# Kernel tuning notes

Hardware: AMD Instinct MI355X
Metric: run time of the kernel (lower is better)

The kernel has to match this reference:

```python
import jax, jax.numpy as jnp
import numpy as np

NEG_INF = -9.0e15  # matches torch's -9000000000000000.0 mask value
ALPHA = 0.2        # LeakyReLU negative slope from init_kwargs


def setup_inputs() -> dict:
    key = jax.random.key(0)
    k1, k2, k3, k4, k5 = jax.random.split(key, 5)
    B, N, D, A = 64, 128, 128, 1000
    hidden = jax.random.normal(k1, (B, N, D), dtype=jnp.float32)
    adj = jax.random.randint(k2, (B, N, N), 0, 5)  # edge types 0..4 (0 = masked)
    a = jax.random.normal(k3, (D, 4), dtype=jnp.float32) * 0.1  # stacked a_0..a_3
    A_attr_sess = jax.random.uniform(k4, (B, N, A), dtype=jnp.float32)
    attr_embedding = jax.random.normal(k5, (A, D), dtype=jnp.float32)
    return {"hidden": hidden, "adj": adj, "a": a,
            "A_attr_sess": A_attr_sess, "attr_embedding": attr_embedding}


def reference(hidden, adj, a, A_attr_sess, attr_embedding):
    # a_input[b,i,j,:] = leaky_relu(h[b,i,:] * h[b,j,:])  -> [B,N,N,D]
    a_input = jax.nn.leaky_relu(hidden[:, :, None, :] * hidden[:, None, :, :],
                                negative_slope=ALPHA)
    # four edge-type scores in one contraction: [B,N,N,4]
    e = jnp.einsum('bijd,dk->bijk', a_input, a)
    # masked selection by adjacency edge type (later writes override earlier)
    alpha = jnp.full(adj.shape, NEG_INF, dtype=e.dtype)
    alpha = jnp.where(adj == 1, e[..., 0], alpha)
    alpha = jnp.where(adj == 2, e[..., 1], alpha)
    alpha = jnp.where(adj == 3, e[..., 2], alpha)
    alpha = jnp.where(adj == 4, e[..., 3], alpha)
    attn = jax.nn.softmax(alpha, axis=-1)        # [B,N,N]
    output = jnp.einsum('bij,bjd->bid', attn, hidden)  # [B,N,D]
    attr_sess = jnp.einsum('bna,ad->bnd', A_attr_sess, attr_embedding)
    return output, attr_sess
```

## Files before the change

### kernel.cpp

```cpp
#include <hip/hip_runtime.h>

#define BB 64
#define NN 128
#define DD 128
#define AA 1000
#define KPAD 1024
#define NEG_INF (-9.0e15f)

typedef __attribute__((ext_vector_type(8))) short short8;
typedef __attribute__((ext_vector_type(4))) float floatx4;
typedef __attribute__((ext_vector_type(4))) unsigned int uintx4;
typedef __attribute__((ext_vector_type(2))) unsigned int uintx2;

__device__ __forceinline__ float bflo(unsigned int u) { return __uint_as_float(u << 16); }
__device__ __forceinline__ float bfhi(unsigned int u) { return __uint_as_float(u & 0xffff0000u); }
__device__ __forceinline__ unsigned int packbf(float f0, float f1) {
  return (__float_as_uint(f0) >> 16) | (__float_as_uint(f1) & 0xffff0000u);
}
__device__ __forceinline__ unsigned short bf_rne(float f) {
  unsigned int u = __float_as_uint(f);
  return (unsigned short)((u + 0x7fffu + ((u >> 16) & 1u)) >> 16);
}
__device__ __forceinline__ unsigned int packbf_rne(float f0, float f1) {
  return (unsigned int)bf_rne(f0) | ((unsigned int)bf_rne(f1) << 16);
}
__device__ __forceinline__ short8 u2s(uintx4 v) {
  union { uintx4 u; short8 s; } x; x.u = v; return x.s;
}

__global__ __launch_bounds__(256) void prep_kernel(
    const float* __restrict__ hidden, const float* __restrict__ emb,
    unsigned short* __restrict__ ET, unsigned short* __restrict__ HTg)
{
  __shared__ float hsf[NN * 129];
  const int t = threadIdx.x;
  const int bid = blockIdx.x;
  if (bid < BB) {
    const float* hb = hidden + (size_t)bid * NN * DD;
    #pragma unroll
    for (int u = 0; u < 16; ++u) {
      int e = u * 1024 + t * 4;
      float4 v = *reinterpret_cast<const float4*>(hb + e);
      int r = e >> 7, c = e & 127;
      float* d = &hsf[r * 129 + c];
      d[0] = v.x; d[1] = v.y; d[2] = v.z; d[3] = v.w;
    }
    __syncthreads();
    unsigned short* ht16 = HTg + (size_t)bid * NN * DD;
    #pragma unroll
    for (int u = 0; u < 8; ++u) {
      int e = u * 2048 + t * 8;
      int dI = e >> 7, il = e & 127;
      float x[8];
      #pragma unroll
      for (int j = 0; j < 8; ++j) x[j] = hsf[(il + j) * 129 + dI];
      uintx4 o;
      o.x = packbf_rne(x[0], x[1]); o.y = packbf_rne(x[2], x[3]);
      o.z = packbf_rne(x[4], x[5]); o.w = packbf_rne(x[6], x[7]);
      *reinterpret_cast<uintx4*>(ht16 + e) = o;
    }
  } else {
    const int k0 = (bid - BB) * 32;
    #pragma unroll
    for (int u = 0; u < 4; ++u) {
      int e = u * 1024 + t * 4;
      int r = e >> 7, c = e & 127;
      float4 z = {0.f, 0.f, 0.f, 0.f};
      float4 v = (k0 + r < AA)
          ? *reinterpret_cast<const float4*>(emb + (size_t)(k0 + r) * DD + c) : z;
      float* d = &hsf[r * 129 + c];
      d[0] = v.x; d[1] = v.y; d[2] = v.z; d[3] = v.w;
    }
    __syncthreads();
    int c = t >> 1, j0 = (t & 1) * 16;
    float x[16];
    #pragma unroll
    for (int j = 0; j < 16; ++j) x[j] = hsf[(j0 + j) * 129 + c];
    uintx4 o0, o1;
    o0.x = packbf_rne(x[0], x[1]);  o0.y = packbf_rne(x[2], x[3]);
    o0.z = packbf_rne(x[4], x[5]);  o0.w = packbf_rne(x[6], x[7]);
    o1.x = packbf_rne(x[8], x[9]);  o1.y = packbf_rne(x[10], x[11]);
    o1.z = packbf_rne(x[12], x[13]); o1.w = packbf_rne(x[14], x[15]);
    unsigned short* dst = ET + (size_t)c * KPAD + k0 + j0;
    *reinterpret_cast<uintx4*>(dst) = o0;
    *reinterpret_cast<uintx4*>(dst + 8) = o1;
  }
}

struct AttnSmem {
  __align__(16) unsigned short Hs[NN * 128];
  union {
    __align__(16) unsigned short As[4 * 16 * 256];
    struct {
      __align__(16) float Sa[16 * 129];
      __align__(16) unsigned short W[16 * 128];
    } sw;
  } u2;
  __align__(16) float saf[4 * 256];
};

#define BK 64
struct AttrSmem {
  __align__(16) unsigned short ETs[2][DD * BK];
  __align__(16) unsigned short As2[2][16 * BK];
};

union FusedSmem { AttnSmem a; AttrSmem g; };

__device__ __forceinline__ void attn_body(
    AttnSmem& s, const float* __restrict__ hidden,
    const int* __restrict__ adj, const float* __restrict__ amat,
    const unsigned short* __restrict__ HTg, float* __restrict__ out0,
    int wid)
{
  const int t = threadIdx.x;
  const int L = t & 63, w = t >> 6;
  const int lr = L & 15, lq = L >> 4;
  const int b = wid >> 3;
  const int i0 = (wid & 7) * 16;

  const int* adjb = adj + ((size_t)b * NN + i0) * NN;
  int adjv[8];
  #pragma unroll
  for (int nt = 0; nt < 2; ++nt)
    #pragma unroll
    for (int r = 0; r < 4; ++r)
      adjv[nt * 4 + r] = adjb[(lq * 4 + r) * NN + w * 32 + nt * 16 + lr];

  const float* hb = hidden + (size_t)b * NN * DD;
  #pragma unroll
  for (int u = 0; u < 8; ++u) {
    int id = u * 256 + t;
    int r = id >> 4, c = id & 15;
    const float* src = hb + r * 128 + c * 8;
    float4 v0 = *reinterpret_cast<const float4*>(src);
    float4 v1 = *reinterpret_cast<const float4*>(src + 4);
    uintx4 o;
    o.x = packbf_rne(v0.x, v0.y); o.y = packbf_rne(v0.z, v0.w);
    o.z = packbf_rne(v1.x, v1.y); o.w = packbf_rne(v1.z, v1.w);
    *reinterpret_cast<uintx4*>(&s.Hs[r * 128 + ((c ^ (r & 15)) << 3)]) = o;
  }
  {
    float v1 = amat[t], v2 = amat[t + 256];
    int dI = t >> 2, k = t & 3;
    s.saf[k * 256 + dI] = 0.6f * v1;
    s.saf[k * 256 + 128 + dI] = 0.4f * v1;
    s.saf[k * 256 + 64 + dI] = 0.6f * v2;
    s.saf[k * 256 + 192 + dI] = 0.4f * v2;
  }
  __syncthreads();

  #pragma unroll
  for (int u = 0; u < 8; ++u) {
    int id = u * 256 + t;
    int k = id >> 9, ii = (id >> 5) & 15, c = id & 31;
    int srow = i0 + ii;
    int dchunk = c & 15;
    uintx4 hv = *reinterpret_cast<const uintx4*>(
        &s.Hs[srow * 128 + ((dchunk ^ (srow & 15)) << 3)]);
    if (c & 16) {
      hv.x &= 0x7fff7fffu; hv.y &= 0x7fff7fffu;
      hv.z &= 0x7fff7fffu; hv.w &= 0x7fff7fffu;
    }
    const float* sf = &s.saf[k * 256 + c * 8];
    uintx4 o;
    o.x = packbf(bflo(hv.x) * sf[0], bfhi(hv.x) * sf[1]);
    o.y = packbf(bflo(hv.y) * sf[2], bfhi(hv.y) * sf[3]);
    o.z = packbf(bflo(hv.z) * sf[4], bfhi(hv.z) * sf[5]);
    o.w = packbf(bflo(hv.w) * sf[6], bfhi(hv.w) * sf[7]);
    *reinterpret_cast<uintx4*>(&s.u2.As[k * 4096 + ii * 256 + ((c ^ ii) << 3)]) = o;
  }
  __syncthreads();

  floatx4 acc[4][2];
  #pragma unroll
  for (int k = 0; k < 4; ++k)
    #pragma unroll
    for (int nt = 0; nt < 2; ++nt) acc[k][nt] = floatx4{0.f, 0.f, 0.f, 0.f};

  #pragma unroll
  for (int kt = 0; kt < 8; ++kt) {
    int ca = lq + 4 * kt;
    short8 afr[4];
    #pragma unroll
    for (int k = 0; k < 4; ++k)
      afr[k] = *reinterpret_cast<const short8*>(
          &s.u2.As[k * 4096 + lr * 256 + ((ca ^ lr) << 3)]);
    int cb = lq + 4 * (kt & 3);
    short8 bfr[2];
    #pragma unroll
    for (int nt = 0; nt < 2; ++nt) {
      int jrow = w * 32 + nt * 16 + lr;
      uintx4 hv = *reinterpret_cast<const uintx4*>(
          &s.Hs[jrow * 128 + ((cb ^ (jrow & 15)) << 3)]);
      if (kt >= 4) {
        hv.x &= 0x7fff7fffu; hv.y &= 0x7fff7fffu;
        hv.z &= 0x7fff7fffu; hv.w &= 0x7fff7fffu;
      }
      bfr[nt] = u2s(hv);
    }
    #pragma unroll
    for (int k = 0; k < 4; ++k)
      #pragma unroll
      for (int nt = 0; nt < 2; ++nt)
        acc[k][nt] = __builtin_amdgcn_mfma_f32_16x16x32_bf16(
            afr[k], bfr[nt], acc[k][nt], 0, 0, 0);
  }
  __syncthreads();

  short8 pvb[2][4];
  const unsigned short* ht = HTg + (size_t)b * NN * DD;
  #pragma unroll
  for (int nt = 0; nt < 2; ++nt)
    #pragma unroll
    for (int kt = 0; kt < 4; ++kt) {
      int dI = w * 32 + nt * 16 + lr;
      pvb[nt][kt] = *reinterpret_cast<const short8*>(ht + dI * 128 + kt * 32 + lq * 8);
    }

  #pragma unroll
  for (int nt = 0; nt < 2; ++nt)
    #pragma unroll
    for (int r = 0; r < 4; ++r) {
      int ii = lq * 4 + r;
      int j = w * 32 + nt * 16 + lr;
      int ad = adjv[nt * 4 + r];
      float al = NEG_INF;
      al = (ad == 1) ? acc[0][nt][r] : al;
      al = (ad == 2) ? acc[1][nt][r] : al;
      al = (ad == 3) ? acc[2][nt][r] : al;
      al = (ad == 4) ? acc[3][nt][r] : al;
      s.u2.sw.Sa[ii * 129 + j] = al;
    }
  __syncthreads();

  #pragma unroll
  for (int p = 0; p < 4; ++p) {
    int ii = w * 4 + p;
    float a1 = s.u2.sw.Sa[ii * 129 + L];
    float a2 = s.u2.sw.Sa[ii * 129 + 64 + L];
    float m = fmaxf(a1, a2);
    #pragma unroll
    for (int off = 32; off > 0; off >>= 1) m = fmaxf(m, __shfl_xor(m, off, 64));
    float e1 = __expf(fmaxf(a1 - m, -80.f));
    float e2 = __expf(fmaxf(a2 - m, -80.f));
    float ss = e1 + e2;
    #pragma unroll
    for (int off = 32; off > 0; off >>= 1) ss += __shfl_xor(ss, off, 64);
    float inv = 1.f / ss;
    int j2 = L + 64;
    s.u2.sw.W[ii * 128 + (((L >> 3) ^ ii) << 3) + (L & 7)] = bf_rne(e1 * inv);
    s.u2.sw.W[ii * 128 + (((j2 >> 3) ^ ii) << 3) + (j2 & 7)] = bf_rne(e2 * inv);
  }
  __syncthreads();

  floatx4 oacc[2];
  oacc[0] = floatx4{0.f, 0.f, 0.f, 0.f};
  oacc[1] = floatx4{0.f, 0.f, 0.f, 0.f};
  #pragma unroll
  for (int kt = 0; kt < 4; ++kt) {
    int c = lq + 4 * kt;
    short8 wf = *reinterpret_cast<const short8*>(
        &s.u2.sw.W[lr * 128 + ((c ^ lr) << 3)]);
    #pragma unroll
    for (int nt = 0; nt < 2; ++nt)
      oacc[nt] = __builtin_amdgcn_mfma_f32_16x16x32_bf16(
          wf, pvb[nt][kt], oacc[nt], 0, 0, 0);
  }
  float* ob = out0 + ((size_t)b * NN + i0) * DD;
  #pragma unroll
  for (int nt = 0; nt < 2; ++nt)
    #pragma unroll
    for (int r = 0; r < 4; ++r)
      ob[(lq * 4 + r) * DD + w * 32 + nt * 16 + lr] = oacc[nt][r];
}

__device__ __forceinline__ void attr_body(
    AttrSmem& s, const float* __restrict__ Aattr,
    const unsigned short* __restrict__ ET, float* __restrict__ out1,
    int wid)
{
  const int t = threadIdx.x;
  const int L = t & 63, w = t >> 6;
  const int lr = L & 15, lq = L >> 4;
  const int r0 = wid * 16;

  const int ar = t >> 4;
  const int ak = (t & 15) * 4;
  const int ec = t >> 1, ej0 = (t & 1) * 4;
  const float* arow = Aattr + (size_t)(r0 + ar) * AA;
  const unsigned short* erow = ET + (size_t)ec * KPAD;

  float4 paA, paB;
  uintx4 peA[4], peB[4];

#define ATTR_FETCH(PA, PE, IT) do {                                          \
    int kb = (IT) * BK; int k4 = kb + ak;                                    \
    float4 z = {0.f, 0.f, 0.f, 0.f};                                        \
    PA = (k4 < AA) ? *reinterpret_cast<const float4*>(arow + k4) : z;        \
    _Pragma("unroll")                                                        \
    for (int q = 0; q < 4; ++q)                                              \
      PE[q] = *reinterpret_cast<const uintx4*>(erow + kb + (ej0 + q) * 8);   \
  } while (0)

#define ATTR_STAGE(PA, PE, BUF) do {                                         \
    uintx2 o; o.x = packbf(PA.x, PA.y); o.y = packbf(PA.z, PA.w);            \
    int cidx = ak >> 3, half = ak & 7;                                       \
    *reinterpret_cast<uintx2*>(                                              \
        &s.As2[BUF][ar * BK + ((cidx ^ (ar & 7)) << 3) + half]) = o;         \
    _Pragma("unroll")                                                        \
    for (int q = 0; q < 4; ++q)                                              \
      *reinterpret_cast<uintx4*>(                                            \
          &s.ETs[BUF][ec * BK + (((ej0 + q) ^ (ec & 7)) << 3)]) = PE[q];     \
  } while (0)

#define ATTR_COMPUTE(BUF) do {                                               \
    _Pragma("unroll")                                                        \
    for (int ks = 0; ks < 2; ++ks) {                                         \
      int c = lq + 4 * ks;                                                   \
      short8 af = *reinterpret_cast<const short8*>(                          \
          &s.As2[BUF][lr * BK + ((c ^ (lr & 7)) << 3)]);                     \
      _Pragma("unroll")                                                      \
      for (int nt = 0; nt < 2; ++nt) {                                       \
        int n = w * 32 + nt * 16 + lr;                                       \
        short8 bf = *reinterpret_cast<const short8*>(                        \
            &s.ETs[BUF][n * BK + ((c ^ (n & 7)) << 3)]);                     \
        acc[nt] = __builtin_amdgcn_mfma_f32_16x16x32_bf16(                   \
            af, bf, acc[nt], 0, 0, 0);                                       \
      }                                                                      \
    }                                                                        \
  } while (0)

  floatx4 acc[2];
  acc[0] = floatx4{0.f, 0.f, 0.f, 0.f};
  acc[1] = floatx4{0.f, 0.f, 0.f, 0.f};

  ATTR_FETCH(paA, peA, 0);
  ATTR_FETCH(paB, peB, 1);
  for (int ith = 0; ith < 8; ++ith) {
    ATTR_STAGE(paA, peA, 0);
    __syncthreads();
    if (ith < 7) ATTR_FETCH(paA, peA, 2 * ith + 2);
    ATTR_COMPUTE(0);
    ATTR_STAGE(paB, peB, 1);
    __syncthreads();
    if (ith < 7) ATTR_FETCH(paB, peB, 2 * ith + 3);
    ATTR_COMPUTE(1);
  }
#undef ATTR_FETCH
#undef ATTR_STAGE
#undef ATTR_COMPUTE

  float* ob = out1 + (size_t)r0 * DD;
  #pragma unroll
  for (int nt = 0; nt < 2; ++nt)
    #pragma unroll
    for (int r = 0; r < 4; ++r)
      ob[(lq * 4 + r) * DD + w * 32 + nt * 16 + lr] = acc[nt][r];
}

__global__ __launch_bounds__(256, 2) void fused_kernel(
    const float* __restrict__ hidden, const int* __restrict__ adj,
    const float* __restrict__ amat, const float* __restrict__ Aattr,
    const unsigned short* __restrict__ ET, const unsigned short* __restrict__ HTg,
    float* __restrict__ out0, float* __restrict__ out1)
{
  __shared__ FusedSmem sm;
  const int bid = blockIdx.x;
  const int wid = (bid & 7) * 64 + (bid >> 3);
  if (wid & 1) {
    attn_body(sm.a, hidden, adj, amat, HTg, out0, wid);
    __syncthreads();
    attr_body(sm.g, Aattr, ET, out1, wid);
  } else {
    attr_body(sm.g, Aattr, ET, out1, wid);
    __syncthreads();
    attn_body(sm.a, hidden, adj, amat, HTg, out0, wid);
  }
}

extern "C" void kernel_launch(void* const* d_in, const int* in_sizes, int n_in,
                              void* d_out, int out_size, void* d_ws, size_t ws_size,
                              hipStream_t stream) {
  const float* hidden = (const float*)d_in[0];
  const int*   adj    = (const int*)d_in[1];
  const float* amat   = (const float*)d_in[2];
  const float* Aattr  = (const float*)d_in[3];
  const float* emb    = (const float*)d_in[4];

  float* out0 = (float*)d_out;
  float* out1 = out0 + (size_t)BB * NN * DD;

  unsigned short* ET  = (unsigned short*)d_ws;
  unsigned short* HTg = ET + (size_t)DD * KPAD;

  prep_kernel<<<BB + 32, 256, 0, stream>>>(hidden, emb, ET, HTg);
  fused_kernel<<<512, 256, 0, stream>>>(hidden, adj, amat, Aattr, ET, HTg,
                                        out0, out1);
}
```

Before: 104.4 us.

## Split attention and attr GEMM into separate blocks, shrink LDS, pre-swizzle bf16 hidden

The prep kernel now also writes a bf16, pre-swizzled copy of hidden, so attention blocks copy it straight into LDS instead of converting fp32 on the fly. The attention score scratch is halved by processing the four edge-type A-operands in two passes, and B fragments are held in registers across both passes. The attr GEMM now computes 32 rows per block with wider A loads. The fused kernel launches 768 single-purpose blocks instead of 512 blocks that each ran both bodies in sequence. Less LDS and launch_bounds of 3 aim to raise occupancy, at the cost of an extra workspace buffer, more global writes in prep, and an extra barrier in the attention pass.

```diff
diff --git a/kernel.cpp b/kernel.cpp
--- a/kernel.cpp
+++ b/kernel.cpp
@@ -30,7 +30,8 @@
 
 __global__ __launch_bounds__(256) void prep_kernel(
     const float* __restrict__ hidden, const float* __restrict__ emb,
-    unsigned short* __restrict__ ET, unsigned short* __restrict__ HTg)
+    unsigned short* __restrict__ ET, unsigned short* __restrict__ HTg,
+    unsigned short* __restrict__ Hg)
 {
   __shared__ float hsf[NN * 129];
   const int t = threadIdx.x;
@@ -59,6 +60,17 @@
       o.z = packbf_rne(x[4], x[5]); o.w = packbf_rne(x[6], x[7]);
       *reinterpret_cast<uintx4*>(ht16 + e) = o;
     }
+    unsigned short* hg = Hg + (size_t)bid * NN * DD;
+    #pragma unroll
+    for (int u = 0; u < 8; ++u) {
+      int id = u * 256 + t;
+      int r = id >> 4, c = id & 15;
+      const float* src = &hsf[r * 129 + c * 8];
+      uintx4 o;
+      o.x = packbf_rne(src[0], src[1]); o.y = packbf_rne(src[2], src[3]);
+      o.z = packbf_rne(src[4], src[5]); o.w = packbf_rne(src[6], src[7]);
+      *reinterpret_cast<uintx4*>(&hg[r * 128 + ((c ^ (r & 15)) << 3)]) = o;
+    }
   } else {
     const int k0 = (bid - BB) * 32;
     #pragma unroll
@@ -90,7 +102,7 @@
 struct AttnSmem {
   __align__(16) unsigned short Hs[NN * 128];
   union {
-    __align__(16) unsigned short As[4 * 16 * 256];
+    __align__(16) unsigned short As[2 * 16 * 256];
     struct {
       __align__(16) float Sa[16 * 129];
       __align__(16) unsigned short W[16 * 128];
@@ -102,22 +114,21 @@
 #define BK 64
 struct AttrSmem {
   __align__(16) unsigned short ETs[2][DD * BK];
-  __align__(16) unsigned short As2[2][16 * BK];
+  __align__(16) unsigned short As2[2][32 * BK];
 };
 
 union FusedSmem { AttnSmem a; AttrSmem g; };
 
 __device__ __forceinline__ void attn_body(
-    AttnSmem& s, const float* __restrict__ hidden,
-    const int* __restrict__ adj, const float* __restrict__ amat,
-    const unsigned short* __restrict__ HTg, float* __restrict__ out0,
-    int wid)
+    AttnSmem& s, const int* __restrict__ adj, const float* __restrict__ amat,
+    const unsigned short* __restrict__ Hg, const unsigned short* __restrict__ HTg,
+    float* __restrict__ out0, int tile)
 {
   const int t = threadIdx.x;
   const int L = t & 63, w = t >> 6;
   const int lr = L & 15, lq = L >> 4;
-  const int b = wid >> 3;
-  const int i0 = (wid & 7) * 16;
+  const int b = tile >> 3;
+  const int i0 = (tile & 7) * 16;
 
   const int* adjb = adj + ((size_t)b * NN + i0) * NN;
   int adjv[8];
@@ -127,18 +138,12 @@
     for (int r = 0; r < 4; ++r)
       adjv[nt * 4 + r] = adjb[(lq * 4 + r) * NN + w * 32 + nt * 16 + lr];
 
-  const float* hb = hidden + (size_t)b * NN * DD;
+  const unsigned short* hg = Hg + (size_t)b * NN * DD;
   #pragma unroll
   for (int u = 0; u < 8; ++u) {
     int id = u * 256 + t;
-    int r = id >> 4, c = id & 15;
-    const float* src = hb + r * 128 + c * 8;
-    float4 v0 = *reinterpret_cast<const float4*>(src);
-    float4 v1 = *reinterpret_cast<const float4*>(src + 4);
-    uintx4 o;
-    o.x = packbf_rne(v0.x, v0.y); o.y = packbf_rne(v0.z, v0.w);
-    o.z = packbf_rne(v1.x, v1.y); o.w = packbf_rne(v1.z, v1.w);
-    *reinterpret_cast<uintx4*>(&s.Hs[r * 128 + ((c ^ (r & 15)) << 3)]) = o;
+    *reinterpret_cast<uintx4*>(&s.Hs[id * 8]) =
+        *reinterpret_cast<const uintx4*>(hg + id * 8);
   }
   {
     float v1 = amat[t], v2 = amat[t + 256];
@@ -150,27 +155,15 @@
   }
   __syncthreads();
 
-  #pragma unroll
-  for (int u = 0; u < 8; ++u) {
-    int id = u * 256 + t;
-    int k = id >> 9, ii = (id >> 5) & 15, c = id & 31;
-    int srow = i0 + ii;
-    int dchunk = c & 15;
-    uintx4 hv = *reinterpret_cast<const uintx4*>(
-        &s.Hs[srow * 128 + ((dchunk ^ (srow & 15)) << 3)]);
-    if (c & 16) {
-      hv.x &= 0x7fff7fffu; hv.y &= 0x7fff7fffu;
-      hv.z &= 0x7fff7fffu; hv.w &= 0x7fff7fffu;
-    }
-    const float* sf = &s.saf[k * 256 + c * 8];
-    uintx4 o;
-    o.x = packbf(bflo(hv.x) * sf[0], bfhi(hv.x) * sf[1]);
-    o.y = packbf(bflo(hv.y) * sf[2], bfhi(hv.y) * sf[3]);
-    o.z = packbf(bflo(hv.z) * sf[4], bfhi(hv.z) * sf[5]);
-    o.w = packbf(bflo(hv.w) * sf[6], bfhi(hv.w) * sf[7]);
-    *reinterpret_cast<uintx4*>(&s.u2.As[k * 4096 + ii * 256 + ((c ^ ii) << 3)]) = o;
-  }
-  __syncthreads();
+  uintx4 hvq[2][4];
+  #pragma unroll
+  for (int nt = 0; nt < 2; ++nt)
+    #pragma unroll
+    for (int q = 0; q < 4; ++q) {
+      int jrow = w * 32 + nt * 16 + lr;
+      hvq[nt][q] = *reinterpret_cast<const uintx4*>(
+          &s.Hs[jrow * 128 + (((lq + 4 * q) ^ (jrow & 15)) << 3)]);
+    }
 
   floatx4 acc[4][2];
   #pragma unroll
@@ -179,32 +172,52 @@
     for (int nt = 0; nt < 2; ++nt) acc[k][nt] = floatx4{0.f, 0.f, 0.f, 0.f};
 
   #pragma unroll
-  for (int kt = 0; kt < 8; ++kt) {
-    int ca = lq + 4 * kt;
-    short8 afr[4];
-    #pragma unroll
-    for (int k = 0; k < 4; ++k)
-      afr[k] = *reinterpret_cast<const short8*>(
-          &s.u2.As[k * 4096 + lr * 256 + ((ca ^ lr) << 3)]);
-    int cb = lq + 4 * (kt & 3);
-    short8 bfr[2];
-    #pragma unroll
-    for (int nt = 0; nt < 2; ++nt) {
-      int jrow = w * 32 + nt * 16 + lr;
+  for (int kp = 0; kp < 2; ++kp) {
+    if (kp) __syncthreads();
+    #pragma unroll
+    for (int u = 0; u < 4; ++u) {
+      int id = u * 256 + t;
+      int kk = id >> 9, ii = (id >> 5) & 15, c = id & 31;
+      int srow = i0 + ii;
+      int dchunk = c & 15;
       uintx4 hv = *reinterpret_cast<const uintx4*>(
-          &s.Hs[jrow * 128 + ((cb ^ (jrow & 15)) << 3)]);
-      if (kt >= 4) {
+          &s.Hs[srow * 128 + ((dchunk ^ (srow & 15)) << 3)]);
+      if (c & 16) {
         hv.x &= 0x7fff7fffu; hv.y &= 0x7fff7fffu;
         hv.z &= 0x7fff7fffu; hv.w &= 0x7fff7fffu;
       }
-      bfr[nt] = u2s(hv);
-    }
-    #pragma unroll
-    for (int k = 0; k < 4; ++k)
+      const float* sf = &s.saf[(kp * 2 + kk) * 256 + c * 8];
+      uintx4 o;
+      o.x = packbf(bflo(hv.x) * sf[0], bfhi(hv.x) * sf[1]);
+      o.y = packbf(bflo(hv.y) * sf[2], bfhi(hv.y) * sf[3]);
+      o.z = packbf(bflo(hv.z) * sf[4], bfhi(hv.z) * sf[5]);
+      o.w = packbf(bflo(hv.w) * sf[6], bfhi(hv.w) * sf[7]);
+      *reinterpret_cast<uintx4*>(&s.u2.As[kk * 4096 + ii * 256 + ((c ^ ii) << 3)]) = o;
+    }
+    __syncthreads();
+
+    #pragma unroll
+    for (int kt = 0; kt < 8; ++kt) {
+      int ca = lq + 4 * kt;
+      short8 afr[2];
       #pragma unroll
-      for (int nt = 0; nt < 2; ++nt)
-        acc[k][nt] = __builtin_amdgcn_mfma_f32_16x16x32_bf16(
-            afr[k], bfr[nt], acc[k][nt], 0, 0, 0);
+      for (int kk = 0; kk < 2; ++kk)
+        afr[kk] = *reinterpret_cast<const short8*>(
+            &s.u2.As[kk * 4096 + lr * 256 + ((ca ^ lr) << 3)]);
+      #pragma unroll
+      for (int nt = 0; nt < 2; ++nt) {
+        uintx4 hv = hvq[nt][kt & 3];
+        if (kt >= 4) {
+          hv.x &= 0x7fff7fffu; hv.y &= 0x7fff7fffu;
+          hv.z &= 0x7fff7fffu; hv.w &= 0x7fff7fffu;
+        }
+        short8 bfr = u2s(hv);
+        #pragma unroll
+        for (int kk = 0; kk < 2; ++kk)
+          acc[kp * 2 + kk][nt] = __builtin_amdgcn_mfma_f32_16x16x32_bf16(
+              afr[kk], bfr, acc[kp * 2 + kk][nt], 0, 0, 0);
+      }
+    }
   }
   __syncthreads();
 
@@ -277,37 +290,39 @@
 
 __device__ __forceinline__ void attr_body(
     AttrSmem& s, const float* __restrict__ Aattr,
-    const unsigned short* __restrict__ ET, float* __restrict__ out1,
-    int wid)
+    const unsigned short* __restrict__ ET, float* __restrict__ out1, int tile)
 {
   const int t = threadIdx.x;
   const int L = t & 63, w = t >> 6;
   const int lr = L & 15, lq = L >> 4;
-  const int r0 = wid * 16;
-
-  const int ar = t >> 4;
-  const int ak = (t & 15) * 4;
+  const int r0 = tile * 32;
+
+  const int ar = t >> 3;
+  const int ak = (t & 7) * 8;
   const int ec = t >> 1, ej0 = (t & 1) * 4;
   const float* arow = Aattr + (size_t)(r0 + ar) * AA;
   const unsigned short* erow = ET + (size_t)ec * KPAD;
 
-  float4 paA, paB;
+  float4 pa0A, pa1A, pa0B, pa1B;
   uintx4 peA[4], peB[4];
 
-#define ATTR_FETCH(PA, PE, IT) do {                                          \
+#define ATTR_FETCH(P0, P1, PE, IT) do {                                      \
     int kb = (IT) * BK; int k4 = kb + ak;                                    \
     float4 z = {0.f, 0.f, 0.f, 0.f};                                        \
-    PA = (k4 < AA) ? *reinterpret_cast<const float4*>(arow + k4) : z;        \
+    P0 = (k4 < AA) ? *reinterpret_cast<const float4*>(arow + k4) : z;        \
+    P1 = (k4 + 4 < AA) ? *reinterpret_cast<const float4*>(arow + k4 + 4) : z;\
     _Pragma("unroll")                                                        \
     for (int q = 0; q < 4; ++q)                                              \
       PE[q] = *reinterpret_cast<const uintx4*>(erow + kb + (ej0 + q) * 8);   \
   } while (0)
 
-#define ATTR_STAGE(PA, PE, BUF) do {                                         \
-    uintx2 o; o.x = packbf(PA.x, PA.y); o.y = packbf(PA.z, PA.w);            \
-    int cidx = ak >> 3, half = ak & 7;                                       \
-    *reinterpret_cast<uintx2*>(                                              \
-        &s.As2[BUF][ar * BK + ((cidx ^ (ar & 7)) << 3) + half]) = o;         \
+#define ATTR_STAGE(P0, P1, PE, BUF) do {                                     \
+    uintx4 o;                                                                \
+    o.x = packbf(P0.x, P0.y); o.y = packbf(P0.z, P0.w);                      \
+    o.z = packbf(P1.x, P1.y); o.w = packbf(P1.z, P1.w);                      \
+    int ac = t & 7;                                                          \
+    *reinterpret_cast<uintx4*>(                                              \
+        &s.As2[BUF][ar * BK + ((ac ^ (ar & 7)) << 3)]) = o;                  \
     _Pragma("unroll")                                                        \
     for (int q = 0; q < 4; ++q)                                              \
       *reinterpret_cast<uintx4*>(                                            \
@@ -318,33 +333,44 @@
     _Pragma("unroll")                                                        \
     for (int ks = 0; ks < 2; ++ks) {                                         \
       int c = lq + 4 * ks;                                                   \
-      short8 af = *reinterpret_cast<const short8*>(                          \
-          &s.As2[BUF][lr * BK + ((c ^ (lr & 7)) << 3)]);                     \
+      short8 af[2], bf[2];                                                   \
+      _Pragma("unroll")                                                      \
+      for (int mt = 0; mt < 2; ++mt) {                                       \
+        int row = mt * 16 + lr;                                              \
+        af[mt] = *reinterpret_cast<const short8*>(                           \
+            &s.As2[BUF][row * BK + ((c ^ (row & 7)) << 3)]);                 \
+      }                                                                      \
       _Pragma("unroll")                                                      \
       for (int nt = 0; nt < 2; ++nt) {                                       \
         int n = w * 32 + nt * 16 + lr;                                       \
-        short8 bf = *reinterpret_cast<const short8*>(                        \
+        bf[nt] = *reinterpret_cast<const short8*>(                           \
             &s.ETs[BUF][n * BK + ((c ^ (n & 7)) << 3)]);                     \
-        acc[nt] = __builtin_amdgcn_mfma_f32_16x16x32_bf16(                   \
-            af, bf, acc[nt], 0, 0, 0);                                       \
       }                                                                      \
+      _Pragma("unroll")                                                      \
+      for (int mt = 0; mt < 2; ++mt)                                         \
+        _Pragma("unroll")                                                    \
+        for (int nt = 0; nt < 2; ++nt)                                       \
+          acc[mt][nt] = __builtin_amdgcn_mfma_f32_16x16x32_bf16(             \
+              af[mt], bf[nt], acc[mt][nt], 0, 0, 0);                         \
     }                                                                        \
   } while (0)
 
-  floatx4 acc[2];
-  acc[0] = floatx4{0.f, 0.f, 0.f, 0.f};
-  acc[1] = floatx4{0.f, 0.f, 0.f, 0.f};
-
-  ATTR_FETCH(paA, peA, 0);
-  ATTR_FETCH(paB, peB, 1);
+  floatx4 acc[2][2];
+  #pragma unroll
+  for (int mt = 0; mt < 2; ++mt)
+    #pragma unroll
+    for (int nt = 0; nt < 2; ++nt) acc[mt][nt] = floatx4{0.f, 0.f, 0.f, 0.f};
+
+  ATTR_FETCH(pa0A, pa1A, peA, 0);
+  ATTR_FETCH(pa0B, pa1B, peB, 1);
   for (int ith = 0; ith < 8; ++ith) {
-    ATTR_STAGE(paA, peA, 0);
+    ATTR_STAGE(pa0A, pa1A, peA, 0);
     __syncthreads();
-    if (ith < 7) ATTR_FETCH(paA, peA, 2 * ith + 2);
+    if (ith < 7) ATTR_FETCH(pa0A, pa1A, peA, 2 * ith + 2);
     ATTR_COMPUTE(0);
-    ATTR_STAGE(paB, peB, 1);
+    ATTR_STAGE(pa0B, pa1B, peB, 1);
     __syncthreads();
-    if (ith < 7) ATTR_FETCH(paB, peB, 2 * ith + 3);
+    if (ith < 7) ATTR_FETCH(pa0B, pa1B, peB, 2 * ith + 3);
     ATTR_COMPUTE(1);
   }
 #undef ATTR_FETCH
@@ -353,30 +379,26 @@
 
   float* ob = out1 + (size_t)r0 * DD;
   #pragma unroll
-  for (int nt = 0; nt < 2; ++nt)
-    #pragma unroll
-    for (int r = 0; r < 4; ++r)
-      ob[(lq * 4 + r) * DD + w * 32 + nt * 16 + lr] = acc[nt][r];
-}
-
-__global__ __launch_bounds__(256, 2) void fused_kernel(
-    const float* __restrict__ hidden, const int* __restrict__ adj,
-    const float* __restrict__ amat, const float* __restrict__ Aattr,
-    const unsigned short* __restrict__ ET, const unsigned short* __restrict__ HTg,
+  for (int mt = 0; mt < 2; ++mt)
+    #pragma unroll
+    for (int nt = 0; nt < 2; ++nt)
+      #pragma unroll
+      for (int r = 0; r < 4; ++r)
+        ob[(mt * 16 + lq * 4 + r) * DD + w * 32 + nt * 16 + lr] = acc[mt][nt][r];
+}
+
+__global__ __launch_bounds__(256, 3) void fused_kernel(
+    const int* __restrict__ adj, const float* __restrict__ amat,
+    const float* __restrict__ Aattr, const unsigned short* __restrict__ ET,
+    const unsigned short* __restrict__ HTg, const unsigned short* __restrict__ Hg,
     float* __restrict__ out0, float* __restrict__ out1)
 {
   __shared__ FusedSmem sm;
   const int bid = blockIdx.x;
-  const int wid = (bid & 7) * 64 + (bid >> 3);
-  if (wid & 1) {
-    attn_body(sm.a, hidden, adj, amat, HTg, out0, wid);
-    __syncthreads();
-    attr_body(sm.g, Aattr, ET, out1, wid);
-  } else {
-    attr_body(sm.g, Aattr, ET, out1, wid);
-    __syncthreads();
-    attn_body(sm.a, hidden, adj, amat, HTg, out0, wid);
-  }
+  const int wid = (bid & 7) * 96 + (bid >> 3);
+  const int m3 = wid % 3;
+  if (m3 == 2) attr_body(sm.g, Aattr, ET, out1, wid / 3);
+  else         attn_body(sm.a, adj, amat, Hg, HTg, out0, (wid / 3) * 2 + m3);
 }
 
 extern "C" void kernel_launch(void* const* d_in, const int* in_sizes, int n_in,
@@ -393,8 +415,9 @@
 
   unsigned short* ET  = (unsigned short*)d_ws;
   unsigned short* HTg = ET + (size_t)DD * KPAD;
-
-  prep_kernel<<<BB + 32, 256, 0, stream>>>(hidden, emb, ET, HTg);
-  fused_kernel<<<512, 256, 0, stream>>>(hidden, adj, amat, Aattr, ET, HTg,
+  unsigned short* Hg  = HTg + (size_t)BB * NN * DD;
+
+  prep_kernel<<<BB + 32, 256, 0, stream>>>(hidden, emb, ET, HTg, Hg);
+  fused_kernel<<<768, 256, 0, stream>>>(adj, amat, Aattr, ET, HTg, Hg,
                                         out0, out1);
 }
```

Measured after the change: 105.4 us. No clear change (+1.0%).

## Interleave attention phases into attr GEMM pipeline slots with merged shared memory

Applied to the files above, without the earlier changes.

Fuses the two previously serial bodies into one kernel that interleaves attention phases (As build, QK MFMA, select, softmax, PV) between the K-loop stages of the attribute GEMM. The aim is to hide global-load latency and keep the MFMA units busy. Each block now handles 32 attention rows and 32 attr rows, so the grid halves to 256 blocks at one block per CU. Shared memory is merged rather than unioned, which raises LDS use and register pressure, and fewer resident waves could lower latency hiding.

```diff
diff --git a/kernel.cpp b/kernel.cpp
--- a/kernel.cpp
+++ b/kernel.cpp
@@ -5,6 +5,7 @@
 #define DD 128
 #define AA 1000
 #define KPAD 1024
+#define BK 64
 #define NEG_INF (-9.0e15f)
 
 typedef __attribute__((ext_vector_type(8))) short short8;
@@ -87,58 +88,267 @@
   }
 }
 
-struct AttnSmem {
+struct MergedSmem {
   __align__(16) unsigned short Hs[NN * 128];
   union {
-    __align__(16) unsigned short As[4 * 16 * 256];
+    __align__(16) unsigned short As[2 * 16 * 256];
     struct {
       __align__(16) float Sa[16 * 129];
       __align__(16) unsigned short W[16 * 128];
     } sw;
   } u2;
   __align__(16) float saf[4 * 256];
+  __align__(16) unsigned short ETs[2][DD * BK];
+  __align__(16) unsigned short As2[2][32 * BK];
 };
 
-#define BK 64
-struct AttrSmem {
-  __align__(16) unsigned short ETs[2][DD * BK];
-  __align__(16) unsigned short As2[2][16 * BK];
-};
-
-union FusedSmem { AttnSmem a; AttrSmem g; };
-
-__device__ __forceinline__ void attn_body(
-    AttnSmem& s, const float* __restrict__ hidden,
-    const int* __restrict__ adj, const float* __restrict__ amat,
-    const unsigned short* __restrict__ HTg, float* __restrict__ out0,
-    int wid)
+__global__ __launch_bounds__(256, 1) void fused_kernel(
+    const float* __restrict__ hidden, const int* __restrict__ adj,
+    const float* __restrict__ amat, const float* __restrict__ Aattr,
+    const unsigned short* __restrict__ ET, const unsigned short* __restrict__ HTg,
+    float* __restrict__ out0, float* __restrict__ out1)
 {
+  __shared__ MergedSmem s;
   const int t = threadIdx.x;
   const int L = t & 63, w = t >> 6;
   const int lr = L & 15, lq = L >> 4;
-  const int b = wid >> 3;
-  const int i0 = (wid & 7) * 16;
-
-  const int* adjb = adj + ((size_t)b * NN + i0) * NN;
-  int adjv[8];
+  const int bid = blockIdx.x;
+  const int wid = (bid & 7) * 32 + (bid >> 3);
+  const int b = wid >> 2;
+  const int i0A = (wid & 3) * 32;
+  const int i0B = i0A + 16;
+  const int r0 = wid * 32;
+
+  const int ar = t >> 3, ak = (t & 7) * 8;
+  const int ec = t >> 1, ej0 = (t & 1) * 4;
+  const float* arow = Aattr + (size_t)(r0 + ar) * AA;
+  const unsigned short* erow = ET + (size_t)ec * KPAD;
+  float4 pa0[2], pa1[2];
+  uintx4 pe[2][4];
+  floatx4 acc2[2][2];
+  #pragma unroll
+  for (int mt = 0; mt < 2; ++mt)
+    #pragma unroll
+    for (int nt = 0; nt < 2; ++nt) acc2[mt][nt] = floatx4{0.f, 0.f, 0.f, 0.f};
+
+#define AFETCH(SP, IT) do {                                                  \
+    int kb = (IT) * BK; int k4 = kb + ak;                                    \
+    float4 z = {0.f, 0.f, 0.f, 0.f};                                        \
+    pa0[SP] = (k4 < AA) ? *reinterpret_cast<const float4*>(arow + k4) : z;   \
+    pa1[SP] = (k4 + 4 < AA) ? *reinterpret_cast<const float4*>(arow + k4 + 4) : z; \
+    _Pragma("unroll")                                                        \
+    for (int q = 0; q < 4; ++q)                                              \
+      pe[SP][q] = *reinterpret_cast<const uintx4*>(erow + kb + (ej0 + q) * 8); \
+  } while (0)
+
+#define ASTAGE(SP) do {                                                      \
+    uintx4 o;                                                                \
+    o.x = packbf(pa0[SP].x, pa0[SP].y); o.y = packbf(pa0[SP].z, pa0[SP].w);  \
+    o.z = packbf(pa1[SP].x, pa1[SP].y); o.w = packbf(pa1[SP].z, pa1[SP].w);  \
+    int ac = t & 7;                                                          \
+    *reinterpret_cast<uintx4*>(&s.As2[SP][ar * BK + ((ac ^ (ar & 7)) << 3)]) = o; \
+    _Pragma("unroll")                                                        \
+    for (int q = 0; q < 4; ++q)                                              \
+      *reinterpret_cast<uintx4*>(&s.ETs[SP][ec * BK + (((ej0 + q) ^ (ec & 7)) << 3)]) = pe[SP][q]; \
+  } while (0)
+
+#define ACOMPUTE(SP) do {                                                    \
+    _Pragma("unroll")                                                        \
+    for (int ks = 0; ks < 2; ++ks) {                                         \
+      int c = lq + 4 * ks;                                                   \
+      short8 af[2], bfv[2];                                                  \
+      _Pragma("unroll")                                                      \
+      for (int mt = 0; mt < 2; ++mt) {                                       \
+        int row = mt * 16 + lr;                                              \
+        af[mt] = *reinterpret_cast<const short8*>(                           \
+            &s.As2[SP][row * BK + ((c ^ (row & 7)) << 3)]);                  \
+      }                                                                      \
+      _Pragma("unroll")                                                      \
+      for (int nt = 0; nt < 2; ++nt) {                                       \
+        int n = w * 32 + nt * 16 + lr;                                       \
+        bfv[nt] = *reinterpret_cast<const short8*>(                          \
+            &s.ETs[SP][n * BK + ((c ^ (n & 7)) << 3)]);                      \
+      }                                                                      \
+      _Pragma("unroll")                                                      \
+      for (int mt = 0; mt < 2; ++mt)                                         \
+        _Pragma("unroll")                                                    \
+        for (int nt = 0; nt < 2; ++nt)                                       \
+          acc2[mt][nt] = __builtin_amdgcn_mfma_f32_16x16x32_bf16(            \
+              af[mt], bfv[nt], acc2[mt][nt], 0, 0, 0);                       \
+    }                                                                        \
+  } while (0)
+
+  floatx4 acc[4][2];
+  uintx4 hvq[2][4];
+  short8 pvb[2][4];
+
+#define ZACC do {                                                            \
+    _Pragma("unroll")                                                        \
+    for (int k = 0; k < 4; ++k)                                              \
+      _Pragma("unroll")                                                      \
+      for (int nt = 0; nt < 2; ++nt) acc[k][nt] = floatx4{0.f, 0.f, 0.f, 0.f}; \
+  } while (0)
+
+#define HVQHOIST do {                                                        \
+    _Pragma("unroll")                                                        \
+    for (int nt = 0; nt < 2; ++nt)                                           \
+      _Pragma("unroll")                                                      \
+      for (int q = 0; q < 4; ++q) {                                          \
+        int jrow = w * 32 + nt * 16 + lr;                                    \
+        hvq[nt][q] = *reinterpret_cast<const uintx4*>(                       \
+            &s.Hs[jrow * 128 + (((lq + 4 * q) ^ (jrow & 15)) << 3)]);        \
+      }                                                                      \
+  } while (0)
+
+#define ASBUILD(I0, KP) do {                                                 \
+    _Pragma("unroll")                                                        \
+    for (int u = 0; u < 4; ++u) {                                            \
+      int id = u * 256 + t;                                                  \
+      int kk = id >> 9, ii = (id >> 5) & 15, c = id & 31;                    \
+      int srow = (I0) + ii;                                                  \
+      int dchunk = c & 15;                                                   \
+      uintx4 hv = *reinterpret_cast<const uintx4*>(                          \
+          &s.Hs[srow * 128 + ((dchunk ^ (srow & 15)) << 3)]);                \
+      if (c & 16) {                                                          \
+        hv.x &= 0x7fff7fffu; hv.y &= 0x7fff7fffu;                            \
+        hv.z &= 0x7fff7fffu; hv.w &= 0x7fff7fffu;                            \
+      }                                                                      \
+      const float* sf = &s.saf[((KP) * 2 + kk) * 256 + c * 8];               \
+      uintx4 o;                                                              \
+      o.x = packbf(bflo(hv.x) * sf[0], bfhi(hv.x) * sf[1]);                  \
+      o.y = packbf(bflo(hv.y) * sf[2], bfhi(hv.y) * sf[3]);                  \
+      o.z = packbf(bflo(hv.z) * sf[4], bfhi(hv.z) * sf[5]);                  \
+      o.w = packbf(bflo(hv.w) * sf[6], bfhi(hv.w) * sf[7]);                  \
+      *reinterpret_cast<uintx4*>(&s.u2.As[kk * 4096 + ii * 256 + ((c ^ ii) << 3)]) = o; \
+    }                                                                        \
+  } while (0)
+
+#define QKPASS(KP) do {                                                      \
+    _Pragma("unroll")                                                        \
+    for (int kt2 = 0; kt2 < 8; ++kt2) {                                      \
+      int ca = lq + 4 * kt2;                                                 \
+      short8 afr[2];                                                         \
+      _Pragma("unroll")                                                      \
+      for (int kk = 0; kk < 2; ++kk)                                         \
+        afr[kk] = *reinterpret_cast<const short8*>(                          \
+            &s.u2.As[kk * 4096 + lr * 256 + ((ca ^ lr) << 3)]);              \
+      _Pragma("unroll")                                                      \
+      for (int nt = 0; nt < 2; ++nt) {                                       \
+        uintx4 hv = hvq[nt][kt2 & 3];                                        \
+        if (kt2 >= 4) {                                                      \
+          hv.x &= 0x7fff7fffu; hv.y &= 0x7fff7fffu;                          \
+          hv.z &= 0x7fff7fffu; hv.w &= 0x7fff7fffu;                          \
+        }                                                                    \
+        short8 bfr = u2s(hv);                                                \
+        _Pragma("unroll")                                                    \
+        for (int kk = 0; kk < 2; ++kk)                                       \
+          acc[(KP) * 2 + kk][nt] = __builtin_amdgcn_mfma_f32_16x16x32_bf16(  \
+              afr[kk], bfr, acc[(KP) * 2 + kk][nt], 0, 0, 0);                \
+      }                                                                      \
+    }                                                                        \
+  } while (0)
+
+#define SELPH(ADJV) do {                                                     \
+    _Pragma("unroll")                                                        \
+    for (int nt = 0; nt < 2; ++nt)                                           \
+      _Pragma("unroll")                                                      \
+      for (int r = 0; r < 4; ++r) {                                          \
+        int ii = lq * 4 + r;                                                 \
+        int j = w * 32 + nt * 16 + lr;                                       \
+        int ad = ADJV[nt * 4 + r];                                           \
+        float al = NEG_INF;                                                  \
+        al = (ad == 1) ? acc[0][nt][r] : al;                                 \
+        al = (ad == 2) ? acc[1][nt][r] : al;                                 \
+        al = (ad == 3) ? acc[2][nt][r] : al;                                 \
+        al = (ad == 4) ? acc[3][nt][r] : al;                                 \
+        s.u2.sw.Sa[ii * 129 + j] = al;                                       \
+      }                                                                      \
+  } while (0)
+
+#define SMPH do {                                                            \
+    _Pragma("unroll")                                                        \
+    for (int p = 0; p < 4; ++p) {                                            \
+      int ii = w * 4 + p;                                                    \
+      float a1 = s.u2.sw.Sa[ii * 129 + L];                                   \
+      float a2 = s.u2.sw.Sa[ii * 129 + 64 + L];                              \
+      float m = fmaxf(a1, a2);                                               \
+      _Pragma("unroll")                                                      \
+      for (int off = 32; off > 0; off >>= 1) m = fmaxf(m, __shfl_xor(m, off, 64)); \
+      float e1 = __expf(fmaxf(a1 - m, -80.f));                               \
+      float e2 = __expf(fmaxf(a2 - m, -80.f));                               \
+      float ss = e1 + e2;                                                    \
+      _Pragma("unroll")                                                      \
+      for (int off = 32; off > 0; off >>= 1) ss += __shfl_xor(ss, off, 64);  \
+      float inv = 1.f / ss;                                                  \
+      int j2 = L + 64;                                                       \
+      s.u2.sw.W[ii * 128 + (((L >> 3) ^ ii) << 3) + (L & 7)] = bf_rne(e1 * inv); \
+      s.u2.sw.W[ii * 128 + (((j2 >> 3) ^ ii) << 3) + (j2 & 7)] = bf_rne(e2 * inv); \
+    }                                                                        \
+  } while (0)
+
+#define PVPH(I0) do {                                                        \
+    floatx4 oacc0 = floatx4{0.f, 0.f, 0.f, 0.f};                             \
+    floatx4 oacc1 = floatx4{0.f, 0.f, 0.f, 0.f};                             \
+    _Pragma("unroll")                                                        \
+    for (int kt2 = 0; kt2 < 4; ++kt2) {                                      \
+      int c = lq + 4 * kt2;                                                  \
+      short8 wf = *reinterpret_cast<const short8*>(                          \
+          &s.u2.sw.W[lr * 128 + ((c ^ lr) << 3)]);                           \
+      oacc0 = __builtin_amdgcn_mfma_f32_16x16x32_bf16(wf, pvb[0][kt2], oacc0, 0, 0, 0); \
+      oacc1 = __builtin_amdgcn_mfma_f32_16x16x32_bf16(wf, pvb[1][kt2], oacc1, 0, 0, 0); \
+    }                                                                        \
+    float* ob = out0 + ((size_t)b * NN + (I0)) * DD;                         \
+    _Pragma("unroll")                                                        \
+    for (int r = 0; r < 4; ++r) {                                            \
+      ob[(lq * 4 + r) * DD + w * 32 + lr] = oacc0[r];                        \
+      ob[(lq * 4 + r) * DD + w * 32 + 16 + lr] = oacc1[r];                   \
+    }                                                                        \
+  } while (0)
+
+#define SLOT(KT, ...) do {                                                   \
+    __syncthreads();                                                         \
+    if ((KT) < 14) { AFETCH((KT) & 1, (KT) + 2); }                           \
+    ACOMPUTE((KT) & 1);                                                      \
+    __VA_ARGS__                                                              \
+    if ((KT) < 15) { ASTAGE(((KT) + 1) & 1); }                               \
+  } while (0)
+
+  AFETCH(0, 0);
+  AFETCH(1, 1);
+  const int* adjb = adj + (size_t)b * NN * NN;
+  int adjvA[8], adjvB[8];
   #pragma unroll
   for (int nt = 0; nt < 2; ++nt)
     #pragma unroll
-    for (int r = 0; r < 4; ++r)
-      adjv[nt * 4 + r] = adjb[(lq * 4 + r) * NN + w * 32 + nt * 16 + lr];
-
-  const float* hb = hidden + (size_t)b * NN * DD;
-  #pragma unroll
-  for (int u = 0; u < 8; ++u) {
-    int id = u * 256 + t;
-    int r = id >> 4, c = id & 15;
-    const float* src = hb + r * 128 + c * 8;
-    float4 v0 = *reinterpret_cast<const float4*>(src);
-    float4 v1 = *reinterpret_cast<const float4*>(src + 4);
-    uintx4 o;
-    o.x = packbf_rne(v0.x, v0.y); o.y = packbf_rne(v0.z, v0.w);
-    o.z = packbf_rne(v1.x, v1.y); o.w = packbf_rne(v1.z, v1.w);
-    *reinterpret_cast<uintx4*>(&s.Hs[r * 128 + ((c ^ (r & 15)) << 3)]) = o;
+    for (int r = 0; r < 4; ++r) {
+      int col = w * 32 + nt * 16 + lr;
+      adjvA[nt * 4 + r] = adjb[(i0A + lq * 4 + r) * NN + col];
+      adjvB[nt * 4 + r] = adjb[(i0B + lq * 4 + r) * NN + col];
+    }
+  {
+    const unsigned short* ht = HTg + (size_t)b * NN * DD;
+    #pragma unroll
+    for (int nt = 0; nt < 2; ++nt)
+      #pragma unroll
+      for (int kt2 = 0; kt2 < 4; ++kt2) {
+        int dI = w * 32 + nt * 16 + lr;
+        pvb[nt][kt2] = *reinterpret_cast<const short8*>(ht + dI * 128 + kt2 * 32 + lq * 8);
+      }
+  }
+  {
+    const float* hb = hidden + (size_t)b * NN * DD;
+    #pragma unroll
+    for (int u = 0; u < 8; ++u) {
+      int id = u * 256 + t;
+      int r = id >> 4, c = id & 15;
+      const float* src = hb + r * 128 + c * 8;
+      float4 v0 = *reinterpret_cast<const float4*>(src);
+      float4 v1 = *reinterpret_cast<const float4*>(src + 4);
+      uintx4 o;
+      o.x = packbf_rne(v0.x, v0.y); o.y = packbf_rne(v0.z, v0.w);
+      o.z = packbf_rne(v1.x, v1.y); o.w = packbf_rne(v1.z, v1.w);
+      *reinterpret_cast<uintx4*>(&s.Hs[r * 128 + ((c ^ (r & 15)) << 3)]) = o;
+    }
   }
   {
     float v1 = amat[t], v2 = amat[t + 256];
@@ -148,235 +358,46 @@
     s.saf[k * 256 + 64 + dI] = 0.6f * v2;
     s.saf[k * 256 + 192 + dI] = 0.4f * v2;
   }
-  __syncthreads();
-
-  #pragma unroll
-  for (int u = 0; u < 8; ++u) {
-    int id = u * 256 + t;
-    int k = id >> 9, ii = (id >> 5) & 15, c = id & 31;
-    int srow = i0 + ii;
-    int dchunk = c & 15;
-    uintx4 hv = *reinterpret_cast<const uintx4*>(
-        &s.Hs[srow * 128 + ((dchunk ^ (srow & 15)) << 3)]);
-    if (c & 16) {
-      hv.x &= 0x7fff7fffu; hv.y &= 0x7fff7fffu;
-      hv.z &= 0x7fff7fffu; hv.w &= 0x7fff7fffu;
-    }
-    const float* sf = &s.saf[k * 256 + c * 8];
-    uintx4 o;
-    o.x = packbf(bflo(hv.x) * sf[0], bfhi(hv.x) * sf[1]);
-    o.y = packbf(bflo(hv.y) * sf[2], bfhi(hv.y) * sf[3]);
-    o.z = packbf(bflo(hv.z) * sf[4], bfhi(hv.z) * sf[5]);
-    o.w = packbf(bflo(hv.w) * sf[6], bfhi(hv.w) * sf[7]);
-    *reinterpret_cast<uintx4*>(&s.u2.As[k * 4096 + ii * 256 + ((c ^ ii) << 3)]) = o;
-  }
-  __syncthreads();
-
-  floatx4 acc[4][2];
-  #pragma unroll
-  for (int k = 0; k < 4; ++k)
-    #pragma unroll
-    for (int nt = 0; nt < 2; ++nt) acc[k][nt] = floatx4{0.f, 0.f, 0.f, 0.f};
-
-  #pragma unroll
-  for (int kt = 0; kt < 8; ++kt) {
-    int ca = lq + 4 * kt;
-    short8 afr[4];
-    #pragma unroll
-    for (int k = 0; k < 4; ++k)
-      afr[k] = *reinterpret_cast<const short8*>(
-          &s.u2.As[k * 4096 + lr * 256 + ((ca ^ lr) << 3)]);
-    int cb = lq + 4 * (kt & 3);
-    short8 bfr[2];
-    #pragma unroll
-    for (int nt = 0; nt < 2; ++nt) {
-      int jrow = w * 32 + nt * 16 + lr;
-      uintx4 hv = *reinterpret_cast<const uintx4*>(
-          &s.Hs[jrow * 128 + ((cb ^ (jrow & 15)) << 3)]);
-      if (kt >= 4) {
-        hv.x &= 0x7fff7fffu; hv.y &= 0x7fff7fffu;
-        hv.z &= 0x7fff7fffu; hv.w &= 0x7fff7fffu;
-      }
-      bfr[nt] = u2s(hv);
-    }
-    #pragma unroll
-    for (int k = 0; k < 4; ++k)
-      #pragma unroll
-      for (int nt = 0; nt < 2; ++nt)
-        acc[k][nt] = __builtin_amdgcn_mfma_f32_16x16x32_bf16(
-            afr[k], bfr[nt], acc[k][nt], 0, 0, 0);
-  }
-  __syncthreads();
-
-  short8 pvb[2][4];
-  const unsigned short* ht = HTg + (size_t)b * NN * DD;
-  #pragma unroll
-  for (int nt = 0; nt < 2; ++nt)
-    #pragma unroll
-    for (int kt = 0; kt < 4; ++kt) {
-      int dI = w * 32 + nt * 16 + lr;
-      pvb[nt][kt] = *reinterpret_cast<const short8*>(ht + dI * 128 + kt * 32 + lq * 8);
-    }
-
-  #pragma unroll
-  for (int nt = 0; nt < 2; ++nt)
-    #pragma unroll
-    for (int r = 0; r < 4; ++r) {
-      int ii = lq * 4 + r;
-      int j = w * 32 + nt * 16 + lr;
-      int ad = adjv[nt * 4 + r];
-      float al = NEG_INF;
-      al = (ad == 1) ? acc[0][nt][r] : al;
-      al = (ad == 2) ? acc[1][nt][r] : al;
-      al = (ad == 3) ? acc[2][nt][r] : al;
-      al = (ad == 4) ? acc[3][nt][r] : al;
-      s.u2.sw.Sa[ii * 129 + j] = al;
-    }
-  __syncthreads();
-
-  #pragma unroll
-  for (int p = 0; p < 4; ++p) {
-    int ii = w * 4 + p;
-    float a1 = s.u2.sw.Sa[ii * 129 + L];
-    float a2 = s.u2.sw.Sa[ii * 129 + 64 + L];
-    float m = fmaxf(a1, a2);
-    #pragma unroll
-    for (int off = 32; off > 0; off >>= 1) m = fmaxf(m, __shfl_xor(m, off, 64));
-    float e1 = __expf(fmaxf(a1 - m, -80.f));
-    float e2 = __expf(fmaxf(a2 - m, -80.f));
-    float ss = e1 + e2;
-    #pragma unroll
-    for (int off = 32; off > 0; off >>= 1) ss += __shfl_xor(ss, off, 64);
-    float inv = 1.f / ss;
-    int j2 = L + 64;
-    s.u2.sw.W[ii * 128 + (((L >> 3) ^ ii) << 3) + (L & 7)] = bf_rne(e1 * inv);
-    s.u2.sw.W[ii * 128 + (((j2 >> 3) ^ ii) << 3) + (j2 & 7)] = bf_rne(e2 * inv);
-  }
-  __syncthreads();
-
-  floatx4 oacc[2];
-  oacc[0] = floatx4{0.f, 0.f, 0.f, 0.f};
-  oacc[1] = floatx4{0.f, 0.f, 0.f, 0.f};
-  #pragma unroll
-  for (int kt = 0; kt < 4; ++kt) {
-    int c = lq + 4 * kt;
-    short8 wf = *reinterpret_cast<const short8*>(
-        &s.u2.sw.W[lr * 128 + ((c ^ lr) << 3)]);
-    #pragma unroll
-    for (int nt = 0; nt < 2; ++nt)
-      oacc[nt] = __builtin_amdgcn_mfma_f32_16x16x32_bf16(
-          wf, pvb[nt][kt], oacc[nt], 0, 0, 0);
-  }
-  float* ob = out0 + ((size_t)b * NN + i0) * DD;
-  #pragma unroll
-  for (int nt = 0; nt < 2; ++nt)
-    #pragma unroll
-    for (int r = 0; r < 4; ++r)
-      ob[(lq * 4 + r) * DD + w * 32 + nt * 16 + lr] = oacc[nt][r];
-}
-
-__device__ __forceinline__ void attr_body(
-    AttrSmem& s, const float* __restrict__ Aattr,
-    const unsigned short* __restrict__ ET, float* __restrict__ out1,
-    int wid)
-{
-  const int t = threadIdx.x;
-  const int L = t & 63, w = t >> 6;
-  const int lr = L & 15, lq = L >> 4;
-  const int r0 = wid * 16;
-
-  const int ar = t >> 4;
-  const int ak = (t & 15) * 4;
-  const int ec = t >> 1, ej0 = (t & 1) * 4;
-  const float* arow = Aattr + (size_t)(r0 + ar) * AA;
-  const unsigned short* erow = ET + (size_t)ec * KPAD;
-
-  float4 paA, paB;
-  uintx4 peA[4], peB[4];
-
-#define ATTR_FETCH(PA, PE, IT) do {                                          \
-    int kb = (IT) * BK; int k4 = kb + ak;                                    \
-    float4 z = {0.f, 0.f, 0.f, 0.f};                                        \
-    PA = (k4 < AA) ? *reinterpret_cast<const float4*>(arow + k4) : z;        \
-    _Pragma("unroll")                                                        \
-    for (int q = 0; q < 4; ++q)                                              \
-      PE[q] = *reinterpret_cast<const uintx4*>(erow + kb + (ej0 + q) * 8);   \
-  } while (0)
-
-#define ATTR_STAGE(PA, PE, BUF) do {                                         \
-    uintx2 o; o.x = packbf(PA.x, PA.y); o.y = packbf(PA.z, PA.w);            \
-    int cidx = ak >> 3, half = ak & 7;                                       \
-    *reinterpret_cast<uintx2*>(                                              \
-        &s.As2[BUF][ar * BK + ((cidx ^ (ar & 7)) << 3) + half]) = o;         \
-    _Pragma("unroll")                                                        \
-    for (int q = 0; q < 4; ++q)                                              \
-      *reinterpret_cast<uintx4*>(                                            \
-          &s.ETs[BUF][ec * BK + (((ej0 + q) ^ (ec & 7)) << 3)]) = PE[q];     \
-  } while (0)
-
-#define ATTR_COMPUTE(BUF) do {                                               \
-    _Pragma("unroll")                                                        \
-    for (int ks = 0; ks < 2; ++ks) {                                         \
-      int c = lq + 4 * ks;                                                   \
-      short8 af = *reinterpret_cast<const short8*>(                          \
-          &s.As2[BUF][lr * BK + ((c ^ (lr & 7)) << 3)]);                     \
-      _Pragma("unroll")                                                      \
-      for (int nt = 0; nt < 2; ++nt) {                                       \
-        int n = w * 32 + nt * 16 + lr;                                       \
-        short8 bf = *reinterpret_cast<const short8*>(                        \
-            &s.ETs[BUF][n * BK + ((c ^ (n & 7)) << 3)]);                     \
-        acc[nt] = __builtin_amdgcn_mfma_f32_16x16x32_bf16(                   \
-            af, bf, acc[nt], 0, 0, 0);                                       \
-      }                                                                      \
-    }                                                                        \
-  } while (0)
-
-  floatx4 acc[2];
-  acc[0] = floatx4{0.f, 0.f, 0.f, 0.f};
-  acc[1] = floatx4{0.f, 0.f, 0.f, 0.f};
-
-  ATTR_FETCH(paA, peA, 0);
-  ATTR_FETCH(paB, peB, 1);
-  for (int ith = 0; ith < 8; ++ith) {
-    ATTR_STAGE(paA, peA, 0);
-    __syncthreads();
-    if (ith < 7) ATTR_FETCH(paA, peA, 2 * ith + 2);
-    ATTR_COMPUTE(0);
-    ATTR_STAGE(paB, peB, 1);
-    __syncthreads();
-    if (ith < 7) ATTR_FETCH(paB, peB, 2 * ith + 3);
-    ATTR_COMPUTE(1);
-  }
-#undef ATTR_FETCH
-#undef ATTR_STAGE
-#undef ATTR_COMPUTE
+  ZACC;
+  ASTAGE(0);
+
+  SLOT(0,  { HVQHOIST; ASBUILD(i0A, 0); });
+  SLOT(1,  { QKPASS(0); });
+  SLOT(2,  { ASBUILD(i0A, 1); });
+  SLOT(3,  { QKPASS(1); });
+  SLOT(4,  { SELPH(adjvA); });
+  SLOT(5,  { SMPH; });
+  SLOT(6,  { PVPH(i0A); ZACC; });
+  SLOT(7,  { ASBUILD(i0B, 0); });
+  SLOT(8,  { QKPASS(0); });
+  SLOT(9,  { ASBUILD(i0B, 1); });
+  SLOT(10, { QKPASS(1); });
+  SLOT(11, { SELPH(adjvB); });
+  SLOT(12, { SMPH; });
+  SLOT(13, { PVPH(i0B); });
+  SLOT(14, {});
+  SLOT(15, {});
 
   float* ob = out1 + (size_t)r0 * DD;
   #pragma unroll
-  for (int nt = 0; nt < 2; ++nt)
-    #pragma unroll
-    for (int r = 0; r < 4; ++r)
-      ob[(lq * 4 + r) * DD + w * 32 + nt * 16 + lr] = acc[nt][r];
-}
-
-__global__ __launch_bounds__(256, 2) void fused_kernel(
-    const float* __restrict__ hidden, const int* __restrict__ adj,
-    const float* __restrict__ amat, const float* __restrict__ Aattr,
-    const unsigned short* __restrict__ ET, const unsigned short* __restrict__ HTg,
-    float* __restrict__ out0, float* __restrict__ out1)
-{
-  __shared__ FusedSmem sm;
-  const int bid = blockIdx.x;
-  const int wid = (bid & 7) * 64 + (bid >> 3);
-  if (wid & 1) {
-    attn_body(sm.a, hidden, adj, amat, HTg, out0, wid);
-    __syncthreads();
-    attr_body(sm.g, Aattr, ET, out1, wid);
-  } else {
-    attr_body(sm.g, Aattr, ET, out1, wid);
-    __syncthreads();
-    attn_body(sm.a, hidden, adj, amat, HTg, out0, wid);
-  }
+  for (int mt = 0; mt < 2; ++mt)
+    #pragma unroll
+    for (int nt = 0; nt < 2; ++nt)
+      #pragma unroll
+      for (int r = 0; r < 4; ++r)
+        ob[(mt * 16 + lq * 4 + r) * DD + w * 32 + nt * 16 + lr] = acc2[mt][nt][r];
+
+#undef AFETCH
+#undef ASTAGE
+#undef ACOMPUTE
+#undef ZACC
+#undef HVQHOIST
+#undef ASBUILD
+#undef QKPASS
+#undef SELPH
+#undef SMPH
+#undef PVPH
+#undef SLOT
 }
 
 extern "C" void kernel_launch(void* const* d_in, const int* in_sizes, int n_in,
@@ -395,6 +416,6 @@
   unsigned short* HTg = ET + (size_t)DD * KPAD;
 
   prep_kernel<<<BB + 32, 256, 0, stream>>>(hidden, emb, ET, HTg);
-  fused_kernel<<<512, 256, 0, stream>>>(hidden, adj, amat, Aattr, ET, HTg,
+  fused_kernel<<<256, 256, 0, stream>>>(hidden, adj, amat, Aattr, ET, HTg,
                                         out0, out1);
 }
```

Measured after the change: 106.1 us. No clear change (+1.6%).
